# Optimization experiments

Hardware: AMD Instinct MI355X
Metric: run time of the kernel (lower is better)

The kernel has to match this reference:

```python
import jax, jax.numpy as jnp
import numpy as np

N = 50000        # num nodes
E = 800000       # num edges (avg degree 16)
NFEAT = 128
NHID = 128
NCLASS = 64


def setup_inputs() -> dict:
    key = jax.random.key(0)
    k0, k1, k2, k3 = jax.random.split(key, 4)
    x = jax.random.normal(k0, (N, NFEAT), dtype=jnp.float32)
    edge_index = jax.random.randint(k1, (2, E), 0, N)
    edge_weight = jnp.ones((E,), dtype=jnp.float32)
    # GCNConv linear weights (glorot-ish uniform), biases zero
    s1 = 1.0 / np.sqrt(NFEAT)
    W1 = jax.random.uniform(k2, (NFEAT, NHID), jnp.float32, -s1, s1)
    b1 = jnp.zeros((NHID,), jnp.float32)
    s2 = 1.0 / np.sqrt(NHID)
    W2 = jax.random.uniform(k3, (NHID, NCLASS), jnp.float32, -s2, s2)
    b2 = jnp.zeros((NCLASS,), jnp.float32)
    return {"x": x, "edge_index": edge_index, "edge_weight": edge_weight,
            "W1": W1, "b1": b1, "W2": W2, "b2": b2}


def reference(x, edge_index, edge_weight, W1, b1, W2, b2):
    n = x.shape[0]
    # add self loops (fill_value = 1.0), as GCNConv(add_self_loops=True)
    loops = jnp.arange(n)
    ei = jnp.concatenate([edge_index, jnp.stack([loops, loops])], axis=1)
    ew = jnp.concatenate([edge_weight, jnp.ones((n,), x.dtype)])
    row, col = ei[0], ei[1]
    # symmetric gcn normalization: D^-1/2 A D^-1/2
    deg = jax.ops.segment_sum(ew, col, num_segments=n)
    dinv = jnp.where(deg > 0, jax.lax.rsqrt(deg), 0.0)
    norm = dinv[row] * ew * dinv[col]        # [E+N]

    def conv(h, W, b):
        h = h @ W                                   # [N, F_out]
        msg = norm[:, None] * h[row]                # gather + scale, [E+N, F_out]
        return jax.ops.segment_sum(msg, col, num_segments=n) + b

    h = jax.nn.relu(conv(x, W1, b1))  # dropout p=0.0 -> identity
    out = conv(h, W2, b2)
    # F.normalize(p=2, dim=-1)
    nrm = jnp.linalg.norm(out, axis=-1, keepdims=True)
    return out / jnp.maximum(nrm, 1e-12)
```

## Files before the change

### kernel.cpp

```cpp
#include <hip/hip_runtime.h>

#define NF 128
#define NC 64
#define SLICES 64

typedef short bf16x8 __attribute__((ext_vector_type(8)));
typedef float f32x4 __attribute__((ext_vector_type(4)));

__device__ __forceinline__ unsigned f2bf(float f) {
    unsigned u = __float_as_uint(f);
    return (u + 0x7FFFu + ((u >> 16) & 1u)) >> 16;
}
__device__ __forceinline__ float bf2f(unsigned h) { return __uint_as_float(h << 16); }

__global__ __launch_bounds__(256) void prep_fused(const int* __restrict__ col,
                                                  unsigned short* __restrict__ eoff16,
                                                  unsigned short* __restrict__ C16,
                                                  const float* __restrict__ W1,
                                                  const float* __restrict__ W2,
                                                  unsigned short* __restrict__ Wt1,
                                                  unsigned short* __restrict__ Wt2,
                                                  const float* __restrict__ X,
                                                  unsigned* __restrict__ Xb2,
                                                  int N, int E, int SL, int nh,
                                                  int CRB, int WTB, int XCB) {
    __shared__ unsigned hist[12544];
    const int b = blockIdx.x;
    const int tid = threadIdx.x;
    if (b < CRB) {
        const int j = b >> 1;
        const int h = b & 1;
        const int nlo = h * nh;
        const int nhi = min(N, nlo + nh);
        const int words = (nhi - nlo + 1) >> 1;
        for (int i = tid; i < words; i += 256) hist[i] = 0;
        __syncthreads();
        const int e0 = j * SL, e1 = min(E, e0 + SL);
        for (int e = e0 + tid; e < e1; e += 256) {
            int c = col[e];
            if (c >= nlo && c < nhi) {
                int cl = c - nlo;
                unsigned sh = (cl & 1) * 16;
                unsigned old = atomicAdd(&hist[cl >> 1], 1u << sh);
                eoff16[e] = (unsigned short)((old >> sh) & 0xffffu);
            }
        }
        __syncthreads();
        unsigned* Cw = (unsigned*)(C16 + (size_t)j * N + nlo);
        for (int i = tid; i < words; i += 256) Cw[i] = hist[i];
    } else if (b < CRB + WTB) {
        int i = (b - CRB) * 256 + tid;
        if (i < 128 * 128) {
            int k = i >> 7, n = i & 127;
            Wt1[n * 128 + k] = (unsigned short)f2bf(W1[i]);
        } else {
            int j = i - 128 * 128;
            if (j < 128 * 64) {
                int k = j >> 6, n = j & 63;
                Wt2[n * 128 + k] = (unsigned short)f2bf(W2[j]);
            }
        }
    } else {
        const float4* X4 = (const float4*)X;
        uint2* O = (uint2*)Xb2;
        int items = N * 32;
        for (int i = (b - CRB - WTB) * 256 + tid; i < items; i += XCB * 256) {
            float4 v = X4[i];
            O[i] = make_uint2(f2bf(v.x) | (f2bf(v.y) << 16),
                              f2bf(v.z) | (f2bf(v.w) << 16));
        }
    }
}

__global__ __launch_bounds__(256) void scanCB(unsigned short* __restrict__ C16,
                                              int* __restrict__ excl,
                                              int* __restrict__ bsum, int N) {
    __shared__ int sh[256];
    int t = threadIdx.x;
    int n = blockIdx.x * 256 + t;
    int run = 0;
    if (n < N) {
#pragma unroll 4
        for (int j = 0; j < SLICES; ++j) {
            size_t idx = (size_t)j * N + n;
            int v = C16[idx];
            C16[idx] = (unsigned short)run;
            run += v;
        }
    }
    sh[t] = run;
    __syncthreads();
    for (int off = 1; off < 256; off <<= 1) {
        int x = (t >= off) ? sh[t - off] : 0;
        __syncthreads();
        sh[t] += x;
        __syncthreads();
    }
    int incl = sh[t];
    if (t == 255) bsum[blockIdx.x] = incl;
    if (n < N) excl[n] = incl - run;
}

__global__ void scan_sums(int* __restrict__ bsum, int nb) {
    int run = 0;
    for (int i = 0; i < nb; ++i) { int v = bsum[i]; bsum[i] = run; run += v; }
    bsum[nb] = run;
}

__global__ __launch_bounds__(256) void scan_add(int* __restrict__ excl,
                                                const int* __restrict__ bsum,
                                                int N, int nb) {
    int i = blockIdx.x * 256 + threadIdx.x;
    if (i < N) excl[i] += bsum[i >> 8];
    if (i == 0) excl[N] = bsum[nb];
}

__global__ __launch_bounds__(256) void scatter_gemm1_fused(const int* __restrict__ row,
                                                           const int* __restrict__ col,
                                                           const float* __restrict__ ew,
                                                           const int* __restrict__ rowPtr,
                                                           const unsigned short* __restrict__ Coff16,
                                                           const unsigned short* __restrict__ eoff16,
                                                           unsigned* __restrict__ csru,
                                                           const unsigned short* __restrict__ Xb,
                                                           const unsigned short* __restrict__ Wt1,
                                                           unsigned short* __restrict__ H1c,
                                                           int N, int E, int SL, int SB) {
    __shared__ char XsB[16384];
    __shared__ char WsB[32768];
    const int tid = threadIdx.x;
    if ((int)blockIdx.x < SB) {
        const int j = blockIdx.x >> 3;
        const int sub = blockIdx.x & 7;
        const int e0 = j * SL, e1 = min(E, e0 + SL);
        const int per = ((e1 - e0) + 7) >> 3;
        const int lo = min(e1, e0 + sub * per);
        const int hi = min(e1, lo + per);
        const unsigned short* Crow = Coff16 + (size_t)j * N;
        for (int e = lo + tid; e < hi; e += 256) {
            int c = col[e];
            int idx = rowPtr[c] + (int)Crow[c] + (int)eoff16[e];
            csru[idx] = ((unsigned)row[e] << 16) | f2bf(ew[e]);
        }
        return;
    }
    const int bm0 = ((int)blockIdx.x - SB) * 64;
    {
        int r = tid >> 2, q4 = (tid & 3) * 4;
        const uint4* src = (const uint4*)(Xb + (size_t)min(bm0 + r, N - 1) * 128);
#pragma unroll
        for (int qq = 0; qq < 4; ++qq) {
            int kb = (q4 + qq) * 16;
            *(uint4*)(XsB + r * 256 + (kb ^ ((r & 7) << 4))) = src[q4 + qq];
        }
    }
    {
        const uint4* src = (const uint4*)Wt1;
#pragma unroll
        for (int t = 0; t < 8; ++t) {
            int i = t * 256 + tid;
            int n = i >> 4, kb = (i & 15) * 16;
            *(uint4*)(WsB + n * 256 + (kb ^ ((n & 7) << 4))) = src[i];
        }
    }
    __syncthreads();
    const int w = tid >> 6, l = tid & 63;
    const int lr = l & 15, lg = l >> 4;
    f32x4 acc[8] = {};
#pragma unroll
    for (int kk = 0; kk < 4; ++kk) {
        int r = w * 16 + lr;
        bf16x8 a = *(const bf16x8*)(XsB + r * 256 + ((kk * 64 + lg * 16) ^ ((r & 7) << 4)));
        bf16x8 b[8];
#pragma unroll
        for (int nt = 0; nt < 8; ++nt) {
            int n = nt * 16 + lr;
            b[nt] = *(const bf16x8*)(WsB + n * 256 + ((kk * 64 + lg * 16) ^ ((n & 7) << 4)));
        }
#pragma unroll
        for (int nt = 0; nt < 8; ++nt)
            acc[nt] = __builtin_amdgcn_mfma_f32_16x16x32_bf16(a, b[nt], acc[nt], 0, 0, 0);
    }
#pragma unroll
    for (int reg = 0; reg < 4; ++reg) {
        int node = bm0 + w * 16 + lg * 4 + reg;
        if (node < N) {
#pragma unroll
            for (int nt = 0; nt < 8; ++nt)
                H1c[((size_t)(nt >> 1) * N + node) * 32 + (nt & 1) * 16 + lr] =
                    (unsigned short)f2bf(acc[nt][reg]);
        }
    }
}

__global__ __launch_bounds__(256) void gemm2_mfma(const unsigned short* __restrict__ A,
                                                  const unsigned short* __restrict__ Wt2,
                                                  unsigned short* __restrict__ H, int N) {
    __shared__ char XsB[32768];
    __shared__ char WsB[16384];
    const int tid = threadIdx.x;
    const int bm0 = blockIdx.x * 128;
    {
        int k16 = tid & 15, r0 = tid >> 4;
        for (int it = 0; it < 8; ++it) {
            int r = it * 16 + r0;
            int node = min(bm0 + r, N - 1);
            uint4 g = *(const uint4*)(A + (size_t)node * 128 + k16 * 8);
            *(uint4*)(XsB + r * 256 + ((k16 * 16) ^ ((r & 7) << 4))) = g;
        }
    }
    {
        const uint4* src = (const uint4*)Wt2;
        for (int t = 0; t < 4; ++t) {
            int i = t * 256 + tid;
            int n = i >> 4, kb = (i & 15) * 16;
            *(uint4*)(WsB + n * 256 + (kb ^ ((n & 7) << 4))) = src[i];
        }
    }
    __syncthreads();
    const int w = tid >> 6, l = tid & 63;
    const int lr = l & 15, lg = l >> 4;
    f32x4 acc[2][4] = {};
#pragma unroll
    for (int kk = 0; kk < 4; ++kk) {
        bf16x8 a[2], b[4];
#pragma unroll
        for (int mt = 0; mt < 2; ++mt) {
            int r = w * 32 + mt * 16 + lr;
            a[mt] = *(const bf16x8*)(XsB + r * 256 + ((kk * 64 + lg * 16) ^ ((r & 7) << 4)));
        }
#pragma unroll
        for (int nt = 0; nt < 4; ++nt) {
            int n = nt * 16 + lr;
            b[nt] = *(const bf16x8*)(WsB + n * 256 + ((kk * 64 + lg * 16) ^ ((n & 7) << 4)));
        }
#pragma unroll
        for (int mt = 0; mt < 2; ++mt)
#pragma unroll
            for (int nt = 0; nt < 4; ++nt)
                acc[mt][nt] = __builtin_amdgcn_mfma_f32_16x16x32_bf16(a[mt], b[nt], acc[mt][nt], 0, 0, 0);
    }
#pragma unroll
    for (int mt = 0; mt < 2; ++mt)
#pragma unroll
        for (int reg = 0; reg < 4; ++reg) {
            int node = bm0 + w * 32 + mt * 16 + lg * 4 + reg;
            if (node < N) {
#pragma unroll
                for (int nt = 0; nt < 4; ++nt)
                    H[(size_t)node * 64 + nt * 16 + lr] = (unsigned short)f2bf(acc[mt][nt][reg]);
            }
        }
}

__global__ __launch_bounds__(256) void deg_dinv_kernel(const int* __restrict__ rowPtr,
                                                       const unsigned* __restrict__ csru,
                                                       float* __restrict__ dinv, int N) {
    int idx = blockIdx.x * 256 + threadIdx.x;
    int n = idx >> 4, l = idx & 15;
    if (n >= N) return;
    int beg = rowPtr[n], end = rowPtr[n + 1];
    float s = 0.f;
    for (int i = beg + l; i < end; i += 16) s += bf2f(csru[i] & 0xffffu);
#pragma unroll
    for (int off = 8; off; off >>= 1) s += __shfl_xor(s, off, 16);
    if (l == 0) dinv[n] = rsqrtf(s + 1.0f);
}

__global__ __launch_bounds__(256) void norm_w_kernel(unsigned* __restrict__ csru,
                                                     const float* __restrict__ dinv, int E) {
    int i = blockIdx.x * 256 + threadIdx.x;
    if (i >= E) return;
    unsigned p = csru[i];
    float w = bf2f(p & 0xffffu) * dinv[p >> 16];
    csru[i] = (p & 0xffff0000u) | f2bf(w);
}

__global__ __launch_bounds__(256) void agg1_plane(const int* __restrict__ rowPtr,
                                                  const unsigned* __restrict__ csru,
                                                  const unsigned* __restrict__ P,
                                                  const float* __restrict__ dinv,
                                                  const float2* __restrict__ b2,
                                                  unsigned* __restrict__ out1,
                                                  int N, int c) {
    int n = (blockIdx.x * 256 + threadIdx.x) >> 4;
    int l = threadIdx.x & 15;
    if (n >= N) return;
    float dn = dinv[n];
    float accx = 0.f, accy = 0.f;
    int beg = rowPtr[n], end = rowPtr[n + 1];
    int j = beg;
    for (; j + 4 <= end; j += 4) {
        unsigned p0 = csru[j + 0], p1 = csru[j + 1], p2 = csru[j + 2], p3 = csru[j + 3];
        unsigned v0 = P[(size_t)(p0 >> 16) * 16 + l];
        unsigned v1 = P[(size_t)(p1 >> 16) * 16 + l];
        unsigned v2 = P[(size_t)(p2 >> 16) * 16 + l];
        unsigned v3 = P[(size_t)(p3 >> 16) * 16 + l];
        float w0 = bf2f(p0 & 0xffffu), w1 = bf2f(p1 & 0xffffu);
        float w2 = bf2f(p2 & 0xffffu), w3 = bf2f(p3 & 0xffffu);
        accx += w0 * bf2f(v0 & 0xffffu); accy += w0 * bf2f(v0 >> 16);
        accx += w1 * bf2f(v1 & 0xffffu); accy += w1 * bf2f(v1 >> 16);
        accx += w2 * bf2f(v2 & 0xffffu); accy += w2 * bf2f(v2 >> 16);
        accx += w3 * bf2f(v3 & 0xffffu); accy += w3 * bf2f(v3 >> 16);
    }
    for (; j < end; ++j) {
        unsigned p = csru[j];
        float w = bf2f(p & 0xffffu);
        unsigned v = P[(size_t)(p >> 16) * 16 + l];
        accx += w * bf2f(v & 0xffffu); accy += w * bf2f(v >> 16);
    }
    unsigned hv = P[(size_t)n * 16 + l];
    float2 bb = b2[c * 16 + l];
    float s = dn * dn;
    float ox = fmaxf(fmaf(dn, accx, s * bf2f(hv & 0xffffu)) + bb.x, 0.f);
    float oy = fmaxf(fmaf(dn, accy, s * bf2f(hv >> 16)) + bb.y, 0.f);
    out1[(size_t)n * 64 + c * 16 + l] = f2bf(ox) | (f2bf(oy) << 16);
}

__global__ __launch_bounds__(256) void agg_gather2(const int* __restrict__ rowPtr,
                                                   const unsigned* __restrict__ csru,
                                                   const unsigned* __restrict__ H3u,
                                                   const float* __restrict__ dinv,
                                                   const float2* __restrict__ b2,
                                                   float2* __restrict__ out2, int N) {
    int n = (blockIdx.x * 256 + threadIdx.x) >> 5;
    int l = threadIdx.x & 31;
    if (n >= N) return;
    float dn = dinv[n];
    float accx = 0.f, accy = 0.f;
    int beg = rowPtr[n], end = rowPtr[n + 1];
    int j = beg;
    for (; j + 4 <= end; j += 4) {
        unsigned p0 = csru[j + 0], p1 = csru[j + 1], p2 = csru[j + 2], p3 = csru[j + 3];
        unsigned v0 = H3u[(size_t)(p0 >> 16) * 32 + l];
        unsigned v1 = H3u[(size_t)(p1 >> 16) * 32 + l];
        unsigned v2 = H3u[(size_t)(p2 >> 16) * 32 + l];
        unsigned v3 = H3u[(size_t)(p3 >> 16) * 32 + l];
        float w0 = bf2f(p0 & 0xffffu), w1 = bf2f(p1 & 0xffffu);
        float w2 = bf2f(p2 & 0xffffu), w3 = bf2f(p3 & 0xffffu);
        accx += w0 * bf2f(v0 & 0xffffu); accy += w0 * bf2f(v0 >> 16);
        accx += w1 * bf2f(v1 & 0xffffu); accy += w1 * bf2f(v1 >> 16);
        accx += w2 * bf2f(v2 & 0xffffu); accy += w2 * bf2f(v2 >> 16);
        accx += w3 * bf2f(v3 & 0xffffu); accy += w3 * bf2f(v3 >> 16);
    }
    for (; j < end; ++j) {
        unsigned p = csru[j];
        float w = bf2f(p & 0xffffu);
        unsigned v = H3u[(size_t)(p >> 16) * 32 + l];
        accx += w * bf2f(v & 0xffffu); accy += w * bf2f(v >> 16);
    }
    unsigned hv = H3u[(size_t)n * 32 + l];
    float2 bb = b2[l];
    float s = dn * dn;
    float vx = fmaf(dn, accx, s * bf2f(hv & 0xffffu)) + bb.x;
    float vy = fmaf(dn, accy, s * bf2f(hv >> 16)) + bb.y;
    float ss = vx * vx + vy * vy;
#pragma unroll
    for (int off = 16; off; off >>= 1) ss += __shfl_xor(ss, off, 64);
    float scale = 1.0f / fmaxf(sqrtf(ss), 1e-12f);
    out2[(size_t)n * 32 + l] = make_float2(vx * scale, vy * scale);
}

extern "C" void kernel_launch(void* const* d_in, const int* in_sizes, int n_in,
                              void* d_out, int out_size, void* d_ws, size_t ws_size,
                              hipStream_t stream) {
    const float* x  = (const float*)d_in[0];
    const int*   ei = (const int*)d_in[1];
    const float* ew = (const float*)d_in[2];
    const float* W1 = (const float*)d_in[3];
    const float* b1 = (const float*)d_in[4];
    const float* W2 = (const float*)d_in[5];
    const float* b2 = (const float*)d_in[6];
    float* out = (float*)d_out;
    const int N = in_sizes[0] / NF;
    const int E = in_sizes[2];
    const int* row = ei;
    const int* col = ei + E;
    const int NB2 = (N + 255) / 256;
    const int SL = (E + SLICES - 1) / SLICES;
    const int nh = (N + 1) / 2;

    char* ws = (char*)d_ws;
    size_t off = 0;
    auto take = [&](size_t bytes) {
        char* p = ws + off;
        off = (off + bytes + 255) & ~(size_t)255;
        return p;
    };
    float* dinv   = (float*)take((size_t)N * 4);
    int*   rowPtr = (int*)  take((size_t)(N + 1) * 4);
    unsigned short* eoff16 = (unsigned short*)take((size_t)E * 2);
    int*   bsum   = (int*)  take((size_t)(NB2 + 1) * 4);
    unsigned short* C16    = (unsigned short*)take((size_t)SLICES * N * 2);
    unsigned* csru = (unsigned*)take((size_t)E * 4);
    unsigned short* Xb   = (unsigned short*)take((size_t)N * NF * 2);
    unsigned short* H1c  = (unsigned short*)take((size_t)N * NF * 2);
    unsigned short* relu = (unsigned short*)take((size_t)N * NF * 2);
    unsigned short* Wt1  = (unsigned short*)take(128 * 128 * 2);
    unsigned short* Wt2  = (unsigned short*)take(64 * 128 * 2);
    unsigned short* H3 = H1c;

    const int CRB = 2 * SLICES, WTB = 96, XCB = 1024;
    prep_fused<<<CRB + WTB + XCB, 256, 0, stream>>>(col, eoff16, C16, W1, W2, Wt1, Wt2,
                                                    x, (unsigned*)Xb, N, E, SL, nh,
                                                    CRB, WTB, XCB);

    scanCB<<<NB2, 256, 0, stream>>>(C16, rowPtr, bsum, N);
    scan_sums<<<1, 1, 0, stream>>>(bsum, NB2);
    scan_add<<<(N + 255) / 256, 256, 0, stream>>>(rowPtr, bsum, N, NB2);

    const int SB = 8 * SLICES;
    const int GB = (N + 63) / 64;
    scatter_gemm1_fused<<<SB + GB, 256, 0, stream>>>(row, col, ew, rowPtr, C16, eoff16,
                                                     csru, Xb, Wt1, H1c, N, E, SL, SB);

    deg_dinv_kernel<<<(N * 16 + 255) / 256, 256, 0, stream>>>(rowPtr, csru, dinv, N);
    norm_w_kernel<<<(E + 255) / 256, 256, 0, stream>>>(csru, dinv, E);

    for (int c = 0; c < 4; ++c) {
        agg1_plane<<<(N * 16 + 255) / 256, 256, 0, stream>>>(
            rowPtr, csru, (const unsigned*)(H1c + (size_t)c * N * 32), dinv,
            (const float2*)b1, (unsigned*)relu, N, c);
    }

    gemm2_mfma<<<(N + 127) / 128, 256, 0, stream>>>(relu, Wt2, H3, N);
    agg_gather2<<<(N * 32 + 255) / 256, 256, 0, stream>>>(rowPtr, csru, (const unsigned*)H3,
                                                          dinv, (const float2*)b2,
                                                          (float2*)out, N);
}
```

Baseline: 181.8 us.

## Replace four-plane layer-1 aggregation with single row-major gather, fold norm into gathers

The first GEMM now writes H1 row-major instead of four 32-column planes. A single agg_gather1 kernel, using a full wavefront per node with two half-waves over alternating edges, replaces the four per-plane aggregation launches. The separate norm_w pass that rewrote csru weights is removed, and dinv[src] is multiplied in on the fly in both gather kernels. This saves launches, one pass over csru and repeated index reads, at the cost of extra dinv lookups per edge and a different cache footprint, since the planes were meant to keep the gathered working set small.

```diff
diff --git a/kernel.cpp b/kernel.cpp
--- a/kernel.cpp
+++ b/kernel.cpp
@@ -124,7 +124,7 @@
                                                            unsigned* __restrict__ csru,
                                                            const unsigned short* __restrict__ Xb,
                                                            const unsigned short* __restrict__ Wt1,
-                                                           unsigned short* __restrict__ H1c,
+                                                           unsigned short* __restrict__ H,
                                                            int N, int E, int SL, int SB) {
     __shared__ char XsB[16384];
     __shared__ char WsB[32768];
@@ -187,8 +187,7 @@
         if (node < N) {
 #pragma unroll
             for (int nt = 0; nt < 8; ++nt)
-                H1c[((size_t)(nt >> 1) * N + node) * 32 + (nt & 1) * 16 + lr] =
-                    (unsigned short)f2bf(acc[nt][reg]);
+                H[(size_t)node * 128 + nt * 16 + lr] = (unsigned short)f2bf(acc[nt][reg]);
         }
     }
 }
@@ -267,54 +266,48 @@
     if (l == 0) dinv[n] = rsqrtf(s + 1.0f);
 }
 
-__global__ __launch_bounds__(256) void norm_w_kernel(unsigned* __restrict__ csru,
-                                                     const float* __restrict__ dinv, int E) {
-    int i = blockIdx.x * 256 + threadIdx.x;
-    if (i >= E) return;
-    unsigned p = csru[i];
-    float w = bf2f(p & 0xffffu) * dinv[p >> 16];
-    csru[i] = (p & 0xffff0000u) | f2bf(w);
-}
-
-__global__ __launch_bounds__(256) void agg1_plane(const int* __restrict__ rowPtr,
-                                                  const unsigned* __restrict__ csru,
-                                                  const unsigned* __restrict__ P,
-                                                  const float* __restrict__ dinv,
-                                                  const float2* __restrict__ b2,
-                                                  unsigned* __restrict__ out1,
-                                                  int N, int c) {
-    int n = (blockIdx.x * 256 + threadIdx.x) >> 4;
-    int l = threadIdx.x & 15;
+__global__ __launch_bounds__(256) void agg_gather1(const int* __restrict__ rowPtr,
+                                                   const unsigned* __restrict__ csru,
+                                                   const uint2* __restrict__ H1u2,
+                                                   const float* __restrict__ dinv,
+                                                   const float4* __restrict__ b4,
+                                                   uint2* __restrict__ out1, int N) {
+    int n = (blockIdx.x * 256 + threadIdx.x) >> 6;
+    int l = threadIdx.x & 63;
     if (n >= N) return;
-    float dn = dinv[n];
-    float accx = 0.f, accy = 0.f;
+    const int half = l >> 5, sub = l & 31;
+    float a0 = 0.f, a1 = 0.f, a2 = 0.f, a3 = 0.f;
     int beg = rowPtr[n], end = rowPtr[n + 1];
-    int j = beg;
-    for (; j + 4 <= end; j += 4) {
-        unsigned p0 = csru[j + 0], p1 = csru[j + 1], p2 = csru[j + 2], p3 = csru[j + 3];
-        unsigned v0 = P[(size_t)(p0 >> 16) * 16 + l];
-        unsigned v1 = P[(size_t)(p1 >> 16) * 16 + l];
-        unsigned v2 = P[(size_t)(p2 >> 16) * 16 + l];
-        unsigned v3 = P[(size_t)(p3 >> 16) * 16 + l];
-        float w0 = bf2f(p0 & 0xffffu), w1 = bf2f(p1 & 0xffffu);
-        float w2 = bf2f(p2 & 0xffffu), w3 = bf2f(p3 & 0xffffu);
-        accx += w0 * bf2f(v0 & 0xffffu); accy += w0 * bf2f(v0 >> 16);
-        accx += w1 * bf2f(v1 & 0xffffu); accy += w1 * bf2f(v1 >> 16);
-        accx += w2 * bf2f(v2 & 0xffffu); accy += w2 * bf2f(v2 >> 16);
-        accx += w3 * bf2f(v3 & 0xffffu); accy += w3 * bf2f(v3 >> 16);
-    }
-    for (; j < end; ++j) {
-        unsigned p = csru[j];
-        float w = bf2f(p & 0xffffu);
-        unsigned v = P[(size_t)(p >> 16) * 16 + l];
-        accx += w * bf2f(v & 0xffffu); accy += w * bf2f(v >> 16);
-    }
-    unsigned hv = P[(size_t)n * 16 + l];
-    float2 bb = b2[c * 16 + l];
-    float s = dn * dn;
-    float ox = fmaxf(fmaf(dn, accx, s * bf2f(hv & 0xffffu)) + bb.x, 0.f);
-    float oy = fmaxf(fmaf(dn, accy, s * bf2f(hv >> 16)) + bb.y, 0.f);
-    out1[(size_t)n * 64 + c * 16 + l] = f2bf(ox) | (f2bf(oy) << 16);
+    for (int j = beg; j < end; j += 8) {
+#pragma unroll
+        for (int q = 0; q < 4; ++q) {
+            int e = j + 2 * q + half;
+            unsigned p = e < end ? csru[e] : 0u;
+            int src = p >> 16;
+            float w = e < end ? bf2f(p & 0xffffu) * dinv[src] : 0.f;
+            uint2 v = H1u2[(size_t)src * 32 + sub];
+            a0 += w * bf2f(v.x & 0xffffu);
+            a1 += w * bf2f(v.x >> 16);
+            a2 += w * bf2f(v.y & 0xffffu);
+            a3 += w * bf2f(v.y >> 16);
+        }
+    }
+    a0 += __shfl_xor(a0, 32, 64);
+    a1 += __shfl_xor(a1, 32, 64);
+    a2 += __shfl_xor(a2, 32, 64);
+    a3 += __shfl_xor(a3, 32, 64);
+    if (half == 0) {
+        float dn = dinv[n];
+        float s = dn * dn;
+        uint2 hv = H1u2[(size_t)n * 32 + sub];
+        float4 bb = b4[sub];
+        float o0 = fmaxf(fmaf(dn, a0, s * bf2f(hv.x & 0xffffu)) + bb.x, 0.f);
+        float o1 = fmaxf(fmaf(dn, a1, s * bf2f(hv.x >> 16)) + bb.y, 0.f);
+        float o2 = fmaxf(fmaf(dn, a2, s * bf2f(hv.y & 0xffffu)) + bb.z, 0.f);
+        float o3 = fmaxf(fmaf(dn, a3, s * bf2f(hv.y >> 16)) + bb.w, 0.f);
+        out1[(size_t)n * 32 + sub] = make_uint2(f2bf(o0) | (f2bf(o1) << 16),
+                                                f2bf(o2) | (f2bf(o3) << 16));
+    }
 }
 
 __global__ __launch_bounds__(256) void agg_gather2(const int* __restrict__ rowPtr,
@@ -332,12 +325,15 @@
     int j = beg;
     for (; j + 4 <= end; j += 4) {
         unsigned p0 = csru[j + 0], p1 = csru[j + 1], p2 = csru[j + 2], p3 = csru[j + 3];
-        unsigned v0 = H3u[(size_t)(p0 >> 16) * 32 + l];
-        unsigned v1 = H3u[(size_t)(p1 >> 16) * 32 + l];
-        unsigned v2 = H3u[(size_t)(p2 >> 16) * 32 + l];
-        unsigned v3 = H3u[(size_t)(p3 >> 16) * 32 + l];
-        float w0 = bf2f(p0 & 0xffffu), w1 = bf2f(p1 & 0xffffu);
-        float w2 = bf2f(p2 & 0xffffu), w3 = bf2f(p3 & 0xffffu);
+        int s0 = p0 >> 16, s1 = p1 >> 16, s2 = p2 >> 16, s3 = p3 >> 16;
+        float w0 = bf2f(p0 & 0xffffu) * dinv[s0];
+        float w1 = bf2f(p1 & 0xffffu) * dinv[s1];
+        float w2 = bf2f(p2 & 0xffffu) * dinv[s2];
+        float w3 = bf2f(p3 & 0xffffu) * dinv[s3];
+        unsigned v0 = H3u[(size_t)s0 * 32 + l];
+        unsigned v1 = H3u[(size_t)s1 * 32 + l];
+        unsigned v2 = H3u[(size_t)s2 * 32 + l];
+        unsigned v3 = H3u[(size_t)s3 * 32 + l];
         accx += w0 * bf2f(v0 & 0xffffu); accy += w0 * bf2f(v0 >> 16);
         accx += w1 * bf2f(v1 & 0xffffu); accy += w1 * bf2f(v1 >> 16);
         accx += w2 * bf2f(v2 & 0xffffu); accy += w2 * bf2f(v2 >> 16);
@@ -345,8 +341,9 @@
     }
     for (; j < end; ++j) {
         unsigned p = csru[j];
-        float w = bf2f(p & 0xffffu);
-        unsigned v = H3u[(size_t)(p >> 16) * 32 + l];
+        int s0 = p >> 16;
+        float w = bf2f(p & 0xffffu) * dinv[s0];
+        unsigned v = H3u[(size_t)s0 * 32 + l];
         accx += w * bf2f(v & 0xffffu); accy += w * bf2f(v >> 16);
     }
     unsigned hv = H3u[(size_t)n * 32 + l];
@@ -394,11 +391,11 @@
     unsigned short* C16    = (unsigned short*)take((size_t)SLICES * N * 2);
     unsigned* csru = (unsigned*)take((size_t)E * 4);
     unsigned short* Xb   = (unsigned short*)take((size_t)N * NF * 2);
-    unsigned short* H1c  = (unsigned short*)take((size_t)N * NF * 2);
+    unsigned short* H1   = (unsigned short*)take((size_t)N * NF * 2);
     unsigned short* relu = (unsigned short*)take((size_t)N * NF * 2);
     unsigned short* Wt1  = (unsigned short*)take(128 * 128 * 2);
     unsigned short* Wt2  = (unsigned short*)take(64 * 128 * 2);
-    unsigned short* H3 = H1c;
+    unsigned short* H3 = H1;
 
     const int CRB = 2 * SLICES, WTB = 96, XCB = 1024;
     prep_fused<<<CRB + WTB + XCB, 256, 0, stream>>>(col, eoff16, C16, W1, W2, Wt1, Wt2,
@@ -412,16 +409,13 @@
     const int SB = 8 * SLICES;
     const int GB = (N + 63) / 64;
     scatter_gemm1_fused<<<SB + GB, 256, 0, stream>>>(row, col, ew, rowPtr, C16, eoff16,
-                                                     csru, Xb, Wt1, H1c, N, E, SL, SB);
+                                                     csru, Xb, Wt1, H1, N, E, SL, SB);
 
     deg_dinv_kernel<<<(N * 16 + 255) / 256, 256, 0, stream>>>(rowPtr, csru, dinv, N);
-    norm_w_kernel<<<(E + 255) / 256, 256, 0, stream>>>(csru, dinv, E);
-
-    for (int c = 0; c < 4; ++c) {
-        agg1_plane<<<(N * 16 + 255) / 256, 256, 0, stream>>>(
-            rowPtr, csru, (const unsigned*)(H1c + (size_t)c * N * 32), dinv,
-            (const float2*)b1, (unsigned*)relu, N, c);
-    }
+
+    agg_gather1<<<(N * 64 + 255) / 256, 256, 0, stream>>>(rowPtr, csru, (const uint2*)H1,
+                                                          dinv, (const float4*)b1,
+                                                          (uint2*)relu, N);
 
     gemm2_mfma<<<(N + 127) / 128, 256, 0, stream>>>(relu, Wt2, H3, N);
     agg_gather2<<<(N * 32 + 255) / 256, 256, 0, stream>>>(rowPtr, csru, (const unsigned*)H3,
```

Result: no change. 182.3 us (+0.2%).
